# Kernel tuning notes

Hardware: AMD Instinct MI355X
Metric: run time of the kernel (lower is better)

Reference implementation:

```python
import jax, jax.numpy as jnp
import numpy as np
import math

N = 2048          # rows (forced: input_dim_B // 2)
DB = 4096         # input_dim_B
DA = 5120         # input_dim_A
DX2 = DA - DB     # 1024, X2 feature dim
M1, M2 = 8, 4
DK, DV1, DV2 = 64, 64, 64
M = 512           # d_model of trailing encoder layers (nhead=1 inside)
LN_EPS = 1e-5


def setup_inputs() -> dict:
    key = jax.random.key(0)
    ks = jax.random.split(key, 24)
    s = 0.02
    f32 = jnp.float32
    inp = {
        "X1": jax.random.normal(ks[0], (N, DB), f32),
        "X2": jax.random.normal(ks[1], (N, DX2), f32),
        "X3": jax.random.normal(ks[2], (N, DB), f32),
        # Type-A heads (stacked over m1)
        "WQ": jax.random.normal(ks[3], (M1, DA, DK), f32) * s,
        "WK": jax.random.normal(ks[4], (M1, DA, DK), f32) * s,
        "WV": jax.random.normal(ks[5], (M1, DA, DV1), f32) * s,
        # Type-B heads (stacked over m2)
        "WVB": jax.random.normal(ks[6], (M2, DX2, DV2), f32) * s,
        "W_ali": jax.random.normal(ks[7], (DB, DB // 2), f32) * s,
        "W_O": jax.random.normal(ks[8], (M1 * DV1 + M2 * DV2, M), f32) * s,
        # two TransformerEncoderLayers (post-LN, nhead=1, relu FFN), stacked over layer dim
        "enc_Wq": jax.random.normal(ks[9], (2, M, M), f32) * s,
        "enc_Wk": jax.random.normal(ks[10], (2, M, M), f32) * s,
        "enc_Wv": jax.random.normal(ks[11], (2, M, M), f32) * s,
        "enc_bq": jnp.zeros((2, M), f32),
        "enc_bk": jnp.zeros((2, M), f32),
        "enc_bv": jnp.zeros((2, M), f32),
        "enc_Wo": jax.random.normal(ks[12], (2, M, M), f32) * s,
        "enc_bo": jnp.zeros((2, M), f32),
        "enc_ln1_g": jnp.ones((2, M), f32),
        "enc_ln1_b": jnp.zeros((2, M), f32),
        "enc_W1": jax.random.normal(ks[13], (2, M, DV1), f32) * s,
        "enc_b1": jnp.zeros((2, DV1), f32),
        "enc_W2": jax.random.normal(ks[14], (2, DV1, M), f32) * s,
        "enc_b2": jnp.zeros((2, M), f32),
        "enc_ln2_g": jnp.ones((2, M), f32),
        "enc_ln2_b": jnp.zeros((2, M), f32),
    }
    return inp


def _layer_norm(x, g, b):
    mu = jnp.mean(x, axis=-1, keepdims=True)
    var = jnp.mean(jnp.square(x - mu), axis=-1, keepdims=True)
    return (x - mu) * jax.lax.rsqrt(var + LN_EPS) * g + b


def _encoder_layer(x, Wq, bq, Wk, bk, Wv, bv, Wo, bo, g1, b1, W1, bW1, W2, bW2, g2, b2):
    # post-norm TransformerEncoderLayer, nhead=1, dropout in eval mode (off)
    q = x @ Wq + bq
    k = x @ Wk + bk
    v = x @ Wv + bv
    att = jax.nn.softmax((q @ k.T) / math.sqrt(M), axis=-1) @ v
    x = _layer_norm(x + (att @ Wo + bo), g1, b1)
    f = jax.nn.relu(x @ W1 + bW1) @ W2 + bW2
    return _layer_norm(x + f, g2, b2)


def reference(X1, X2, X3, WQ, WK, WV, WVB, W_ali, W_O,
              enc_Wq, enc_bq, enc_Wk, enc_bk, enc_Wv, enc_bv, enc_Wo, enc_bo,
              enc_ln1_g, enc_ln1_b, enc_W1, enc_b1, enc_W2, enc_b2, enc_ln2_g, enc_ln2_b):
    XA = jnp.concatenate([X1, X2], axis=1)  # [N, DA]
    # Type-A heads, batched over m1
    Q = jnp.einsum('nd,hdk->hnk', XA, WQ)
    K = jnp.einsum('nd,hdk->hnk', XA, WK)
    V = jnp.einsum('nd,hdv->hnv', XA, WV)
    scores = jnp.einsum('hnk,hmk->hnm', Q, K) / math.sqrt(DK)
    S = jax.nn.softmax(scores, axis=1)  # torch softmax(dim=0): over query/row axis
    ZA = jnp.einsum('hnm,hmv->hnv', S, V)             # [m1, N, dv1]
    ZA = jnp.transpose(ZA, (1, 0, 2)).reshape(N, M1 * DV1)
    # Type-B heads
    ali = jax.nn.sigmoid(X3) @ W_ali                  # [N, N] (DB//2 == N)
    zb = jnp.einsum('nd,hdv->hnv', X2, WVB)           # [m2, N, dv2]
    ZB = jnp.einsum('nm,hmv->hnv', ali, zb)
    ZB = jnp.transpose(ZB, (1, 0, 2)).reshape(N, M2 * DV2)
    Z = jnp.concatenate([ZA, ZB], axis=1) @ W_O       # [N, M]
    for l in range(2):
        Z = _encoder_layer(Z, enc_Wq[l], enc_bq[l], enc_Wk[l], enc_bk[l],
                           enc_Wv[l], enc_bv[l], enc_Wo[l], enc_bo[l],
                           enc_ln1_g[l], enc_ln1_b[l], enc_W1[l], enc_b1[l],
                           enc_W2[l], enc_b2[l], enc_ln2_g[l], enc_ln2_b[l])
    return Z
```

## Files before the change

### kernel.cpp

```cpp
#include <hip/hip_runtime.h>

#define DEV __device__ __forceinline__

typedef __attribute__((ext_vector_type(4))) float f32x4;
typedef __attribute__((ext_vector_type(8))) short s16x8;

DEV ushort f2b(float f) {
  union { float f; unsigned u; } x; x.f = f;
  unsigned r = (x.u + 0x7FFFu + ((x.u >> 16) & 1u)) >> 16;
  return (ushort)r;
}
DEV float b2f(ushort u) {
  union { unsigned u; float f; } x; x.u = ((unsigned)u) << 16;
  return x.f;
}

DEV void gload16(const ushort* g, ushort* l) {
  __builtin_amdgcn_global_load_lds(
      (const __attribute__((address_space(1))) unsigned int*)g,
      (__attribute__((address_space(3))) unsigned int*)l, 16, 0, 0);
}

struct PtrList { const float* p[4]; };

template<int BM, int BN, int BIAS, int ACT, bool OF, bool OB, int SKX,
         bool CSTAT, bool RSTAT, int NBUF>
__global__ __launch_bounds__(256) void gemm(
    const ushort* __restrict__ A, int lda, long long sA,
    const ushort* __restrict__ B, int ldb, long long sB,
    float* __restrict__ Cf, ushort* __restrict__ Cb, int ldc, long long sC,
    const float* __restrict__ bias, const float* __restrict__ bias2,
    float* __restrict__ pmo, float* __restrict__ pso,
    float scale0, float scale1, int K)
{
  constexpr int WM = BM / 2, WN = BN / 2, FM = WM / 16, FN = WN / 16;
  __shared__ __align__(16) ushort As[NBUF][BM * 64];
  __shared__ __align__(16) ushort Bs[NBUF][BN * 64];
  const int tid = threadIdx.x, l = tid & 63, w = tid >> 6;
  const int wr = w >> 1, wc = w & 1;
  const int gx = gridDim.x, gy = gridDim.y;
  const int nwg = gx * gy;
  const int orig = blockIdx.y * gx + blockIdx.x;
  const int xcd = orig & 7, rest = orig >> 3;
  const int q8 = nwg >> 3, r8 = nwg & 7;
  const int f = (xcd < r8 ? xcd * (q8 + 1) : r8 * (q8 + 1) + (xcd - r8) * q8) + rest;
  int bxr = f / gy;
  const int byy = f - bxr * gy;
  int ks = 0;
  if constexpr (SKX > 1) {
    const int nbx = gx / SKX;
    ks = bxr / nbx; bxr -= ks * nbx;
  }
  const int brow = byy * BM, bcol = bxr * BN;
  const long long z = blockIdx.z;
  A += z * sA + (size_t)ks * K;
  B += z * sB + (size_t)ks * K;
  const int lr = l & 15;
  const int sw = lr & 7, kh = l >> 4;
  f32x4 acc[FM][FN] = {};
  const int nk = K >> 6;

  auto stage = [&](int kt, int buf) {
    const int kof = kt << 6;
#pragma unroll
    for (int i = 0; i < BM / 32; ++i) {
      const int c = i * 256 + tid;
      const int r = c >> 3, k8 = c & 7;
      gload16(A + (size_t)(brow + r) * lda + kof + ((k8 ^ (r & 7)) << 3),
              &As[buf][i * 2048 + w * 512]);
    }
#pragma unroll
    for (int i = 0; i < BN / 32; ++i) {
      const int c = i * 256 + tid;
      const int r = c >> 3, k8 = c & 7;
      gload16(B + (size_t)(bcol + r) * ldb + kof + ((k8 ^ (r & 7)) << 3),
              &Bs[buf][i * 2048 + w * 512]);
    }
  };

  auto compute = [&](int kt, int buf) {
#pragma unroll
    for (int kk = 0; kk < 2; ++kk) {
      const int koff = ((kk * 4 + kh) ^ sw) << 3;
      s16x8 af[FM], bf[FN];
#pragma unroll
      for (int m = 0; m < FM; ++m)
        af[m] = *(const s16x8*)&As[buf][(wr * WM + m * 16 + lr) * 64 + koff];
#pragma unroll
      for (int n = 0; n < FN; ++n)
        bf[n] = *(const s16x8*)&Bs[buf][(wc * WN + n * 16 + lr) * 64 + koff];
#pragma unroll
      for (int m = 0; m < FM; ++m)
#pragma unroll
        for (int n = 0; n < FN; ++n)
          acc[m][n] = __builtin_amdgcn_mfma_f32_16x16x32_bf16(af[m], bf[n], acc[m][n], 0, 0, 0);
    }
  };

  if constexpr (NBUF == 2) {
    stage(0, 0);
    __syncthreads();
    for (int kt = 0; kt < nk - 1; ++kt) {
      stage(kt + 1, (kt + 1) & 1);
      compute(kt, kt & 1);
      __syncthreads();
    }
    compute(nk - 1, (nk - 1) & 1);
  } else {
    for (int kt = 0; kt < nk; ++kt) {
      stage(kt, 0);
      __syncthreads();
      compute(kt, 0);
      __syncthreads();
    }
  }

  if constexpr (OF || OB) {
    const float sc = (z == 0) ? scale0 : scale1;
    const float* bp = (z == 0) ? bias : bias2;
    const int cr = (l >> 4) * 4, cc = l & 15;
#pragma unroll
    for (int m = 0; m < FM; ++m) {
      const int r0 = brow + wr * WM + m * 16 + cr;
#pragma unroll
      for (int n = 0; n < FN; ++n) {
        const int gc = bcol + wc * WN + n * 16 + cc;
        float bc = 0.f;
        if constexpr (BIAS == 1) bc = bp[gc];
#pragma unroll
        for (int j = 0; j < 4; ++j) {
          float v = acc[m][n][j];
          if constexpr (BIAS == 1) v += bc;
          if constexpr (BIAS == 2) v += bp[r0 + j];
          v *= sc;
          if constexpr (ACT == 1) v = fmaxf(v, 0.f);
          const size_t off = (size_t)(r0 + j) * ldc + gc + (size_t)((z * SKX + ks) * sC);
          if constexpr (OF) Cf[off] = v;
          if constexpr (OB) Cb[off] = f2b(v);
        }
      }
    }
  }

  if constexpr (CSTAT) {
    __shared__ float sM[2][2][FN][16], sS[2][2][FN][16];
    float mx[FN], se[FN];
#pragma unroll
    for (int n = 0; n < FN; ++n) {
      float m0 = -3e38f;
#pragma unroll
      for (int m = 0; m < FM; ++m)
#pragma unroll
        for (int j = 0; j < 4; ++j) m0 = fmaxf(m0, acc[m][n][j]);
      float s0 = 0.f;
#pragma unroll
      for (int m = 0; m < FM; ++m)
#pragma unroll
        for (int j = 0; j < 4; ++j) s0 += __expf(acc[m][n][j] - m0);
      mx[n] = m0; se[n] = s0;
    }
#pragma unroll
    for (int o = 16; o <= 32; o <<= 1) {
#pragma unroll
      for (int n = 0; n < FN; ++n) {
        float m2 = __shfl_xor(mx[n], o), s2 = __shfl_xor(se[n], o);
        float M = fmaxf(mx[n], m2);
        se[n] = se[n] * __expf(mx[n] - M) + s2 * __expf(m2 - M);
        mx[n] = M;
      }
    }
    __syncthreads();
    if (l < 16) {
#pragma unroll
      for (int n = 0; n < FN; ++n) { sM[wr][wc][n][l] = mx[n]; sS[wr][wc][n][l] = se[n]; }
    }
    __syncthreads();
    if (wr == 0 && l < 16) {
#pragma unroll
      for (int n = 0; n < FN; ++n) {
        float m1 = sM[0][wc][n][l], m2 = sM[1][wc][n][l];
        float s1 = sS[0][wc][n][l], s2 = sS[1][wc][n][l];
        float M = fmaxf(m1, m2);
        float S = s1 * __expf(m1 - M) + s2 * __expf(m2 - M);
        const int gc = bcol + wc * 32 + n * 16 + l;
        const size_t o = ((size_t)(z * gy + byy)) * 2048 + gc;
        pmo[o] = M; pso[o] = S;
      }
    }
  }

  if constexpr (RSTAT) {
    __shared__ float sRM[2][2][WM], sRS[2][2][WM];
#pragma unroll
    for (int m = 0; m < FM; ++m) {
#pragma unroll
      for (int j = 0; j < 4; ++j) {
        float m0 = -3e38f;
#pragma unroll
        for (int n = 0; n < FN; ++n) m0 = fmaxf(m0, acc[m][n][j]);
        float s0 = 0.f;
#pragma unroll
        for (int n = 0; n < FN; ++n) s0 += __expf(acc[m][n][j] - m0);
#pragma unroll
        for (int o = 1; o <= 8; o <<= 1) {
          float m2 = __shfl_xor(m0, o), s2 = __shfl_xor(s0, o);
          float M = fmaxf(m0, m2);
          s0 = s0 * __expf(m0 - M) + s2 * __expf(m2 - M);
          m0 = M;
        }
        if ((l & 15) == 0) {
          sRM[wr][wc][m * 16 + (l >> 4) * 4 + j] = m0;
          sRS[wr][wc][m * 16 + (l >> 4) * 4 + j] = s0;
        }
      }
    }
    __syncthreads();
    if (wc == 0) {
      float m1 = sRM[wr][0][l], m2 = sRM[wr][1][l];
      float s1 = sRS[wr][0][l], s2 = sRS[wr][1][l];
      float M = fmaxf(m1, m2);
      float S = s1 * __expf(m1 - M) + s2 * __expf(m2 - M);
      const size_t o = (size_t)bxr * 2048 + brow + wr * WM + l;
      pmo[o] = M; pso[o] = S;
    }
  }
}

struct Frag8 { int dummy; };

template<int MH, int NH, bool RA, bool RB>
DEV void phase_read(const ushort* __restrict__ Asb, const ushort* __restrict__ Bsb,
                    int arow, int brw, int kh, int sw,
                    s16x8 (&af)[2][4], s16x8 (&bfh)[2][2][2]) {
  if constexpr (RA) {
#pragma unroll
    for (int kk = 0; kk < 2; ++kk) {
      const int koff = ((kk * 4 + kh) ^ sw) << 3;
#pragma unroll
      for (int m = 0; m < 4; ++m)
        af[kk][m] = *(const s16x8*)&Asb[MH * 8192 + (arow + m * 16) * 64 + koff];
    }
  }
  if constexpr (RB) {
#pragma unroll
    for (int kk = 0; kk < 2; ++kk) {
      const int koff = ((kk * 4 + kh) ^ sw) << 3;
#pragma unroll
      for (int n = 0; n < 2; ++n)
        bfh[NH][kk][n] = *(const s16x8*)&Bsb[NH * 8192 + (brw + n * 16) * 64 + koff];
    }
  }
}

template<int MH, int NH>
DEV void qmfma(const s16x8 (&af)[2][4], const s16x8 (&bfh)[2][2][2],
               f32x4 (&acc)[8][4]) {
#pragma unroll
  for (int kk = 0; kk < 2; ++kk)
#pragma unroll
    for (int m = 0; m < 4; ++m)
#pragma unroll
      for (int n = 0; n < 2; ++n)
        acc[MH * 4 + m][NH * 2 + n] = __builtin_amdgcn_mfma_f32_16x16x32_bf16(
            af[kk][m], bfh[NH][kk][n], acc[MH * 4 + m][NH * 2 + n], 0, 0, 0);
}

DEV void tailwait(int c) {
  if (c == 1) { asm volatile("s_waitcnt vmcnt(4)" ::: "memory"); }
  else if (c == 2) { asm volatile("s_waitcnt vmcnt(0)" ::: "memory"); }
}

template<int NBX>
__global__ __launch_bounds__(512, 2) void gemm256(
    const ushort* __restrict__ A, int lda,
    const ushort* __restrict__ B, int ldb,
    ushort* __restrict__ Cb, int ldc, long long sC, int Kc)
{
  __shared__ __align__(16) ushort As[2][2][8192];
  __shared__ __align__(16) ushort Bs[2][2][8192];
  const int tid = threadIdx.x, l = tid & 63, w = tid >> 6;
  const int wr = w >> 2, wc = w & 3;
  const int gx = gridDim.x, gy = gridDim.y;
  const int nwg = gx * gy;
  const int orig = blockIdx.y * gx + blockIdx.x;
  const int xcd = orig & 7, rest = orig >> 3;
  const int q8 = nwg >> 3, r8 = nwg & 7;
  const int f = (xcd < r8 ? xcd * (q8 + 1) : r8 * (q8 + 1) + (xcd - r8) * q8) + rest;
  int bxr = f / gy;
  const int byy = f - bxr * gy;
  const int ks = bxr / NBX; bxr -= ks * NBX;
  const int brow = byy * 256, bcol = bxr * 256;
  A += (size_t)ks * Kc;
  B += (size_t)ks * Kc;
  const int nk = Kc >> 6;
  const int lr = l & 15, kh = l >> 4, sw = lr & 7;
  const int arow = wr * 64 + lr, brw = wc * 32 + lr;

  const int r0 = tid >> 3, k80 = tid & 7;
  const size_t aoff = (size_t)(brow + r0) * lda + ((k80 ^ (r0 & 7)) << 3);
  const size_t boff = (size_t)(bcol + r0) * ldb + ((k80 ^ (r0 & 7)) << 3);

  f32x4 acc[8][4] = {};
  s16x8 af[2][4];
  s16x8 bfh[2][2][2];

  auto stA = [&](int kt, int buf, int half) {
    if (kt >= nk) return;
    const ushort* s = A + aoff + (size_t)(half * 128) * lda + (kt << 6);
    gload16(s, &As[buf][half][w * 512]);
    gload16(s + (size_t)64 * lda, &As[buf][half][4096 + w * 512]);
  };
  auto stB = [&](int kt, int buf, int half) {
    if (kt >= nk) return;
    const ushort* s = B + boff + (size_t)(half * 128) * ldb + (kt << 6);
    gload16(s, &Bs[buf][half][w * 512]);
    gload16(s + (size_t)64 * ldb, &Bs[buf][half][4096 + w * 512]);
  };

  stA(0, 0, 0); stB(0, 0, 0); stA(0, 0, 1); stB(0, 0, 1);
  stA(1, 1, 0); stB(1, 1, 0);
  asm volatile("s_waitcnt vmcnt(4)" ::: "memory");
  asm volatile("s_barrier" ::: "memory");

#define PH(BUF, MH, NH, RA, RB, STG, TW) do {                                  \
    phase_read<MH, NH, RA, RB>(&As[BUF][0][0], &Bs[BUF][0][0],                 \
                               arow, brw, kh, sw, af, bfh);                    \
    STG;                                                                       \
    asm volatile("s_barrier" ::: "memory");                                    \
    asm volatile("s_waitcnt lgkmcnt(0)" ::: "memory");                         \
    __builtin_amdgcn_sched_barrier(0);                                         \
    __builtin_amdgcn_s_setprio(1);                                             \
    qmfma<MH, NH>(af, bfh, acc);                                               \
    __builtin_amdgcn_s_setprio(0);                                             \
    tailwait(TW);                                                              \
    asm volatile("s_barrier" ::: "memory");                                    \
  } while (0)

  const int NT2 = nk >> 1;
#pragma unroll 1
  for (int j = 0; j < NT2; ++j) {
    const int t1 = 2 * j + 1, t2 = 2 * j + 2, t3 = 2 * j + 3;
    const int tw4 = (t2 < nk) ? 1 : 2;
    const int tw8 = (t2 < nk) ? 1 : 0;
    PH(0, 0, 0, true,  true,  stA(t1, 1, 1), 0);
    PH(0, 0, 1, false, true,  stB(t1, 1, 1), 0);
    PH(0, 1, 0, true,  false, stA(t2, 0, 0), 0);
    PH(0, 1, 1, false, false, stB(t2, 0, 0), tw4);
    PH(1, 0, 0, true,  true,  stA(t2, 0, 1), 0);
    PH(1, 0, 1, false, true,  stB(t2, 0, 1), 0);
    PH(1, 1, 0, true,  false, stA(t3, 1, 0), 0);
    PH(1, 1, 1, false, false, stB(t3, 1, 0), tw8);
  }
#undef PH

  ushort* out = Cb + (size_t)ks * sC;
  const int cr = kh * 4, cc = lr;
#pragma unroll
  for (int mh = 0; mh < 2; ++mh)
#pragma unroll
    for (int m = 0; m < 4; ++m) {
      const int ro = brow + mh * 128 + wr * 64 + m * 16 + cr;
#pragma unroll
      for (int nh = 0; nh < 2; ++nh)
#pragma unroll
        for (int n = 0; n < 2; ++n) {
          const int gc = bcol + nh * 128 + wc * 32 + n * 16 + cc;
#pragma unroll
          for (int j2 = 0; j2 < 4; ++j2)
            out[(size_t)(ro + j2) * ldc + gc] = f2b(acc[mh * 4 + m][nh * 2 + n][j2]);
        }
    }
}

__global__ __launch_bounds__(256) void ffn_fused(
    const ushort* __restrict__ X, const ushort* __restrict__ W1,
    const float* __restrict__ b1, const ushort* __restrict__ W2T,
    const float* __restrict__ b2, float* __restrict__ Y)
{
  __shared__ __align__(16) ushort As[64 * 64];
  __shared__ __align__(16) ushort Bs[64 * 64];
  __shared__ __align__(16) ushort Hs[64 * 64];
  const int tid = threadIdx.x, l = tid & 63, w = tid >> 6;
  const int wr = w >> 1, wc = w & 1;
  const int bx = blockIdx.x, brow = blockIdx.y * 64;
  const int lr = l & 15, g = l >> 4, sw = lr & 7;
  f32x4 acc[2][2] = {};
  for (int kt = 0; kt < 8; ++kt) {
    const int kof = kt << 6;
#pragma unroll
    for (int i = 0; i < 2; ++i) {
      const int c = i * 256 + tid, r = c >> 3, k8 = c & 7;
      gload16(X + (size_t)(brow + r) * 512 + kof + ((k8 ^ (r & 7)) << 3),
              &As[i * 2048 + w * 512]);
    }
#pragma unroll
    for (int i = 0; i < 2; ++i) {
      const int c = i * 256 + tid, r = c >> 3, k8 = c & 7;
      gload16(W1 + (size_t)r * 512 + kof + ((k8 ^ (r & 7)) << 3),
              &Bs[i * 2048 + w * 512]);
    }
    __syncthreads();
#pragma unroll
    for (int kk = 0; kk < 2; ++kk) {
      const int koff = ((kk * 4 + g) ^ sw) << 3;
      s16x8 af[2], bf[2];
#pragma unroll
      for (int m = 0; m < 2; ++m) af[m] = *(const s16x8*)&As[(wr * 32 + m * 16 + lr) * 64 + koff];
#pragma unroll
      for (int n = 0; n < 2; ++n) bf[n] = *(const s16x8*)&Bs[(wc * 32 + n * 16 + lr) * 64 + koff];
#pragma unroll
      for (int m = 0; m < 2; ++m)
#pragma unroll
        for (int n = 0; n < 2; ++n)
          acc[m][n] = __builtin_amdgcn_mfma_f32_16x16x32_bf16(af[m], bf[n], acc[m][n], 0, 0, 0);
    }
    __syncthreads();
  }
#pragma unroll
  for (int m = 0; m < 2; ++m)
#pragma unroll
    for (int n = 0; n < 2; ++n) {
      const int col = wc * 32 + n * 16 + lr;
      const float bb = b1[col];
#pragma unroll
      for (int j = 0; j < 4; ++j) {
        const int row = wr * 32 + m * 16 + g * 4 + j;
        Hs[row * 64 + (((col >> 3) ^ (row & 7)) << 3) + (col & 7)] =
            f2b(fmaxf(acc[m][n][j] + bb, 0.f));
      }
    }
#pragma unroll
  for (int i = 0; i < 2; ++i) {
    const int c = i * 256 + tid, r = c >> 3, k8 = c & 7;
    gload16(W2T + (size_t)(bx * 64 + r) * 64 + ((k8 ^ (r & 7)) << 3),
            &Bs[i * 2048 + w * 512]);
  }
  __syncthreads();
  f32x4 acc2[2][2] = {};
#pragma unroll
  for (int kk = 0; kk < 2; ++kk) {
    const int koff = ((kk * 4 + g) ^ sw) << 3;
    s16x8 af[2], bf[2];
#pragma unroll
    for (int m = 0; m < 2; ++m) af[m] = *(const s16x8*)&Hs[(wr * 32 + m * 16 + lr) * 64 + koff];
#pragma unroll
    for (int n = 0; n < 2; ++n) bf[n] = *(const s16x8*)&Bs[(wc * 32 + n * 16 + lr) * 64 + koff];
#pragma unroll
    for (int m = 0; m < 2; ++m)
#pragma unroll
      for (int n = 0; n < 2; ++n)
        acc2[m][n] = __builtin_amdgcn_mfma_f32_16x16x32_bf16(af[m], bf[n], acc2[m][n], 0, 0, 0);
  }
#pragma unroll
  for (int m = 0; m < 2; ++m)
#pragma unroll
    for (int n = 0; n < 2; ++n) {
      const int gc = bx * 64 + wc * 32 + n * 16 + lr;
      const float bb = b2[gc];
#pragma unroll
      for (int j = 0; j < 4; ++j) {
        const int row = brow + wr * 32 + m * 16 + g * 4 + j;
        Y[(size_t)row * 512 + gc] = acc2[m][n][j] + bb;
      }
    }
}

__global__ __launch_bounds__(256) void pv_fused(
    const ushort* __restrict__ Q, const ushort* __restrict__ K,
    const ushort* __restrict__ Vt, const float* __restrict__ lse,
    ushort* __restrict__ ZAP)
{
  __shared__ __align__(16) ushort Qs[64 * 64];
  __shared__ __align__(16) ushort Ks[2][64 * 64];
  __shared__ __align__(16) ushort Vs[2][64 * 64];
  __shared__ __align__(16) ushort Ps[64 * 64];
  __shared__ float Ls[512];
  const int tid = threadIdx.x, l = tid & 63, w = tid >> 6;
  const int wr = w >> 1, wc = w & 1;
  const int h = blockIdx.z, brow = blockIdx.x * 64, ms = blockIdx.y;
  const int lr = l & 15, g = l >> 4, sw = lr & 7;

  auto stageKV = [&](int mc, int buf) {
#pragma unroll
    for (int i = 0; i < 2; ++i) {
      const int c = i * 256 + tid, r = c >> 3, k8 = c & 7;
      gload16(K + (size_t)(mc * 64 + r) * 512 + h * 64 + ((k8 ^ (r & 7)) << 3),
              &Ks[buf][i * 2048 + w * 512]);
    }
#pragma unroll
    for (int i = 0; i < 2; ++i) {
      const int c = i * 256 + tid, r = c >> 3, k8 = c & 7;
      gload16(Vt + (size_t)(h * 64 + r) * 2048 + mc * 64 + ((k8 ^ (r & 7)) << 3),
              &Vs[buf][i * 2048 + w * 512]);
    }
  };

#pragma unroll
  for (int i = 0; i < 2; ++i) {
    const int c = i * 256 + tid, r = c >> 3, k8 = c & 7;
    gload16(Q + (size_t)(brow + r) * 512 + h * 64 + ((k8 ^ (r & 7)) << 3),
            &Qs[i * 2048 + w * 512]);
  }
  stageKV(ms * 8, 0);
  for (int i = tid; i < 512; i += 256) Ls[i] = lse[h * 2048 + ms * 512 + i];
  __syncthreads();

  s16x8 aq[2][2];
#pragma unroll
  for (int nf = 0; nf < 2; ++nf)
#pragma unroll
    for (int kk = 0; kk < 2; ++kk)
      aq[nf][kk] = *(const s16x8*)&Qs[(wr * 32 + nf * 16 + lr) * 64 + (((kk * 4 + g) ^ sw) << 3)];

  f32x4 zacc[2][2] = {};
  for (int mi = 0; mi < 8; ++mi) {
    const int mc = ms * 8 + mi;
    const int buf = mi & 1;
    if (mi < 7) stageKV(mc + 1, buf ^ 1);
    f32x4 sacc[2][2] = {};
#pragma unroll
    for (int kk = 0; kk < 2; ++kk) {
      const int koff = ((kk * 4 + g) ^ sw) << 3;
      s16x8 bk[2];
#pragma unroll
      for (int mf = 0; mf < 2; ++mf)
        bk[mf] = *(const s16x8*)&Ks[buf][(wc * 32 + mf * 16 + lr) * 64 + koff];
#pragma unroll
      for (int nf = 0; nf < 2; ++nf)
#pragma unroll
        for (int mf = 0; mf < 2; ++mf)
          sacc[nf][mf] = __builtin_amdgcn_mfma_f32_16x16x32_bf16(aq[nf][kk], bk[mf], sacc[nf][mf], 0, 0, 0);
    }
#pragma unroll
    for (int nf = 0; nf < 2; ++nf)
#pragma unroll
      for (int mf = 0; mf < 2; ++mf) {
        const int m_loc = wc * 32 + mf * 16 + lr;
        const float lv = Ls[mi * 64 + m_loc];
#pragma unroll
        for (int j = 0; j < 4; ++j) {
          const int n_loc = wr * 32 + nf * 16 + g * 4 + j;
          Ps[n_loc * 64 + (((m_loc >> 3) ^ (n_loc & 7)) << 3) + (m_loc & 7)] =
              f2b(__expf(sacc[nf][mf][j] - lv));
        }
      }
    __syncthreads();
#pragma unroll
    for (int kk = 0; kk < 2; ++kk) {
      const int koff = ((kk * 4 + g) ^ sw) << 3;
      s16x8 pa[2], bv[2];
#pragma unroll
      for (int nf = 0; nf < 2; ++nf)
        pa[nf] = *(const s16x8*)&Ps[(wr * 32 + nf * 16 + lr) * 64 + koff];
#pragma unroll
      for (int vf = 0; vf < 2; ++vf)
        bv[vf] = *(const s16x8*)&Vs[buf][(wc * 32 + vf * 16 + lr) * 64 + koff];
#pragma unroll
      for (int nf = 0; nf < 2; ++nf)
#pragma unroll
        for (int vf = 0; vf < 2; ++vf)
          zacc[nf][vf] = __builtin_amdgcn_mfma_f32_16x16x32_bf16(pa[nf], bv[vf], zacc[nf][vf], 0, 0, 0);
    }
    __syncthreads();
  }
  ushort* out = ZAP + (size_t)ms * 2048 * 512;
#pragma unroll
  for (int nf = 0; nf < 2; ++nf)
#pragma unroll
    for (int vf = 0; vf < 2; ++vf)
#pragma unroll
      for (int j = 0; j < 4; ++j) {
        const int n = brow + wr * 32 + nf * 16 + g * 4 + j;
        const int col = h * 64 + wc * 32 + vf * 16 + lr;
        out[(size_t)n * 512 + col] = f2b(zacc[nf][vf][j]);
      }
}

template<int NS, int ACT>
__global__ __launch_bounds__(256) void reduceN(const ushort* __restrict__ P, long long sC,
    ushort* __restrict__ out, int cols, int ldout, long long zPoff, long long zOoff,
    int cshift, long long bstride, float scale, int scThresh, int rows,
    const float* __restrict__ bias)
{
  P += blockIdx.z * zPoff; out += blockIdx.z * zOoff;
  const int c4n = cols >> 2;
  const size_t total = (size_t)rows * c4n;
  for (size_t i = (size_t)blockIdx.x * 256 + threadIdx.x; i < total; i += (size_t)gridDim.x * 256) {
    const size_t r = i / c4n;
    const int c4 = (int)(i - r * c4n) << 2;
    float4 s = make_float4(0.f, 0.f, 0.f, 0.f);
#pragma unroll
    for (int k = 0; k < NS; ++k) {
      ushort4 t = *(const ushort4*)(P + (size_t)k * sC + r * cols + c4);
      s.x += b2f(t.x); s.y += b2f(t.y); s.z += b2f(t.z); s.w += b2f(t.w);
    }
    if constexpr (ACT == 1) {
      float4 bb = *(const float4*)(bias + c4);
      s.x = fmaxf(s.x + bb.x, 0.f); s.y = fmaxf(s.y + bb.y, 0.f);
      s.z = fmaxf(s.z + bb.z, 0.f); s.w = fmaxf(s.w + bb.w, 0.f);
    }
    const float sc = (c4 < scThresh) ? scale : 1.f;
    ushort4 o;
    o.x = f2b(s.x * sc); o.y = f2b(s.y * sc); o.z = f2b(s.z * sc); o.w = f2b(s.w * sc);
    const size_t oo = r * ldout + (size_t)(c4 >> cshift) * bstride + (c4 & ((1 << cshift) - 1));
    *(ushort4*)(out + oo) = o;
  }
}

__global__ __launch_bounds__(256) void prep_xab(const float* __restrict__ X1,
    const float* __restrict__ X2, ushort* __restrict__ XAb) {
  const size_t total = (size_t)2048 * 1280;
  for (size_t i = (size_t)blockIdx.x * 256 + threadIdx.x; i < total; i += (size_t)gridDim.x * 256) {
    const size_t r = i / 1280;
    const int c = (int)(i - r * 1280) << 2;
    float4 v = (c < 4096) ? *(const float4*)(X1 + r * 4096 + c)
                          : *(const float4*)(X2 + r * 1024 + (c - 4096));
    ushort4 o; o.x = f2b(v.x); o.y = f2b(v.y); o.z = f2b(v.z); o.w = f2b(v.w);
    *(ushort4*)(XAb + r * 5120 + c) = o;
  }
}

__global__ __launch_bounds__(256) void prep_x3w(const float* __restrict__ X3,
    const float* __restrict__ Wali, ushort* __restrict__ sX3,
    ushort* __restrict__ Walib) {
  const size_t n1 = (size_t)2048 * 1024;
  const size_t n2 = (size_t)4096 * 512;
  const size_t total = n1 + n2;
  for (size_t i = (size_t)blockIdx.x * 256 + threadIdx.x; i < total; i += (size_t)gridDim.x * 256) {
    if (i < n1) {
      const size_t r = i / 1024;
      const int c = (int)(i - r * 1024) << 2;
      float4 v = *(const float4*)(X3 + r * 4096 + c);
      v.x = 1.f / (1.f + __expf(-v.x)); v.y = 1.f / (1.f + __expf(-v.y));
      v.z = 1.f / (1.f + __expf(-v.z)); v.w = 1.f / (1.f + __expf(-v.w));
      ushort4 o; o.x = f2b(v.x); o.y = f2b(v.y); o.z = f2b(v.z); o.w = f2b(v.w);
      *(ushort4*)(sX3 + r * 4096 + c) = o;
    } else {
      const size_t j = i - n1;
      const size_t r = j / 512;
      const int c = (int)(j - r * 512) << 2;
      float4 v = *(const float4*)(Wali + r * 2048 + c);
      ushort4 o; o.x = f2b(v.x); o.y = f2b(v.y); o.z = f2b(v.z); o.w = f2b(v.w);
      *(ushort4*)(Walib + r * 2048 + c) = o;
    }
  }
}

__global__ __launch_bounds__(256) void expconv_row(const float* __restrict__ S,
    const float* __restrict__ pm, const float* __restrict__ ps, ushort* __restrict__ P) {
  const int r = blockIdx.x;
  float m = pm[(size_t)(threadIdx.x & 31) * 2048 + r];
  float s = ps[(size_t)(threadIdx.x & 31) * 2048 + r];
#pragma unroll
  for (int o = 1; o < 32; o <<= 1) {
    float m2 = __shfl_xor(m, o), s2 = __shfl_xor(s, o);
    float M = fmaxf(m, m2);
    s = s * __expf(m - M) + s2 * __expf(m2 - M);
    m = M;
  }
  const float L = m + __logf(s);
  const float* row = S + (size_t)r * 2048;
  ushort* pr = P + (size_t)r * 2048;
  for (int c = threadIdx.x * 4; c < 2048; c += 1024) {
    float4 v = *(const float4*)(row + c);
    ushort4 o4;
    o4.x = f2b(__expf(v.x - L)); o4.y = f2b(__expf(v.y - L));
    o4.z = f2b(__expf(v.z - L)); o4.w = f2b(__expf(v.w - L));
    *(ushort4*)(pr + c) = o4;
  }
}

__global__ __launch_bounds__(256) void colcombine(const float* __restrict__ pm,
    const float* __restrict__ ps, float* __restrict__ lse) {
  const int id = blockIdx.x * 256 + threadIdx.x;
  const int h = id >> 11, c = id & 2047;
  float M = -3e38f;
#pragma unroll
  for (int s = 0; s < 16; ++s) M = fmaxf(M, pm[((size_t)(h * 16 + s)) * 2048 + c]);
  float S = 0.f;
#pragma unroll
  for (int s = 0; s < 16; ++s) {
    size_t o = ((size_t)(h * 16 + s)) * 2048 + c;
    S += ps[o] * __expf(pm[o] - M);
  }
  lse[id] = M + __logf(S);
}

__global__ __launch_bounds__(256) void transpose_conv_multi(PtrList in, int zPerT,
    ushort* __restrict__ out, int R, int C) {
  __shared__ ushort t[32][33];
  const int z = blockIdx.z;
  const float* ip = in.p[z / zPerT] + (size_t)(z % zPerT) * R * C;
  ushort* op = out + (size_t)z * R * C;
  const int r0 = blockIdx.x * 32, c0 = blockIdx.y * 32;
#pragma unroll
  for (int i = 0; i < 4; ++i) {
    int r = r0 + threadIdx.y + i * 8;
    int c = c0 + threadIdx.x;
    float v = (r < R && c < C) ? ip[(size_t)r * C + c] : 0.f;
    t[threadIdx.x][threadIdx.y + i * 8] = f2b(v);
  }
  __syncthreads();
#pragma unroll
  for (int i = 0; i < 4; ++i) {
    int c = c0 + threadIdx.y + i * 8;
    int r = r0 + threadIdx.x;
    if (c < C && r < R) op[(size_t)c * R + r] = t[threadIdx.y + i * 8][threadIdx.x];
  }
}

__global__ __launch_bounds__(256) void transpose_conv_batch(
    const float* __restrict__ WVB, ushort* __restrict__ WVBT,
    const float* __restrict__ W_O, ushort* __restrict__ WOT,
    const float* __restrict__ eW1, ushort* __restrict__ EW1T,
    const float* __restrict__ eW2, ushort* __restrict__ EW2T) {
  __shared__ ushort t[32][33];
  const int b = blockIdx.x;
  const float* ip; ushort* op; int R, C, r0, c0;
  if (b < 256) {
    const int h = b >> 6, loc = b & 63;
    ip = WVB + (size_t)h * 65536; op = WVBT + (size_t)h * 65536;
    R = 1024; C = 64; r0 = (loc & 31) * 32; c0 = (loc >> 5) * 32;
  } else if (b < 640) {
    const int loc = b - 256;
    ip = W_O; op = WOT;
    R = 768; C = 512; r0 = (loc % 24) * 32; c0 = (loc / 24) * 32;
  } else if (b < 704) {
    const int loc = b - 640, lyr = loc >> 5, lo = loc & 31;
    ip = eW1 + (size_t)lyr * 32768; op = EW1T + (size_t)lyr * 32768;
    R = 512; C = 64; r0 = (lo & 15) * 32; c0 = (lo >> 4) * 32;
  } else {
    const int loc = b - 704, lyr = loc >> 5, lo = loc & 31;
    ip = eW2 + (size_t)lyr * 32768; op = EW2T + (size_t)lyr * 32768;
    R = 64; C = 512; r0 = (lo & 1) * 32; c0 = (lo >> 1) * 32;
  }
#pragma unroll
  for (int i = 0; i < 4; ++i) {
    int r = r0 + threadIdx.y + i * 8;
    int c = c0 + threadIdx.x;
    float v = (r < R && c < C) ? ip[(size_t)r * C + c] : 0.f;
    t[threadIdx.x][threadIdx.y + i * 8] = f2b(v);
  }
  __syncthreads();
#pragma unroll
  for (int i = 0; i < 4; ++i) {
    int c = c0 + threadIdx.y + i * 8;
    int r = r0 + threadIdx.x;
    if (c < C && r < R) op[(size_t)c * R + r] = t[threadIdx.y + i * 8][threadIdx.x];
  }
}

__global__ __launch_bounds__(256) void transpose_b16(const ushort* __restrict__ in,
    ushort* __restrict__ out, int R, int C) {
  __shared__ ushort t[32][33];
  const int r0 = blockIdx.x * 32, c0 = blockIdx.y * 32;
#pragma unroll
  for (int i = 0; i < 4; ++i)
    t[threadIdx.x][threadIdx.y + i * 8] = in[(size_t)(r0 + threadIdx.y + i * 8) * C + c0 + threadIdx.x];
  __syncthreads();
#pragma unroll
  for (int i = 0; i < 4; ++i)
    out[(size_t)(c0 + threadIdx.y + i * 8) * R + r0 + threadIdx.x] = t[threadIdx.y + i * 8][threadIdx.x];
}

__global__ __launch_bounds__(256) void ln_add(const float* __restrict__ X,
    const float* __restrict__ Y, const float* __restrict__ g, const float* __restrict__ b,
    float* __restrict__ of, ushort* __restrict__ ob) {
  const int r = blockIdx.x, t = threadIdx.x;
  const size_t base = (size_t)r * 512;
  float v0 = X[base + t] + Y[base + t];
  float v1 = X[base + t + 256] + Y[base + t + 256];
  float s = v0 + v1;
#pragma unroll
  for (int o = 1; o < 64; o <<= 1) s += __shfl_xor(s, o);
  __shared__ float sm[4], sq[4];
  const int l = t & 63, w = t >> 6;
  if (l == 0) sm[w] = s;
  __syncthreads();
  const float mu = (sm[0] + sm[1] + sm[2] + sm[3]) * (1.f / 512.f);
  const float d0 = v0 - mu, d1 = v1 - mu;
  float q = d0 * d0 + d1 * d1;
#pragma unroll
  for (int o = 1; o < 64; o <<= 1) q += __shfl_xor(q, o);
  if (l == 0) sq[w] = q;
  __syncthreads();
  const float var = (sq[0] + sq[1] + sq[2] + sq[3]) * (1.f / 512.f);
  const float rs = rsqrtf(var + 1e-5f);
  const float o0 = d0 * rs * g[t] + b[t];
  const float o1 = d1 * rs * g[t + 256] + b[t + 256];
  if (of) { of[base + t] = o0; of[base + t + 256] = o1; }
  if (ob) { ob[base + t] = f2b(o0); ob[base + t + 256] = f2b(o1); }
}

extern "C" void kernel_launch(void* const* d_in, const int* in_sizes, int n_in,
                              void* d_out, int out_size, void* d_ws, size_t ws_size,
                              hipStream_t stream) {
  (void)in_sizes; (void)n_in; (void)out_size;
  const float* X1   = (const float*)d_in[0];
  const float* X2   = (const float*)d_in[1];
  const float* X3   = (const float*)d_in[2];
  const float* WQ   = (const float*)d_in[3];
  const float* WK   = (const float*)d_in[4];
  const float* WV   = (const float*)d_in[5];
  const float* WVB  = (const float*)d_in[6];
  const float* Wali = (const float*)d_in[7];
  const float* W_O  = (const float*)d_in[8];
  const float* eWq  = (const float*)d_in[9];
  const float* eWk  = (const float*)d_in[10];
  const float* eWv  = (const float*)d_in[11];
  const float* ebq  = (const float*)d_in[12];
  const float* ebk  = (const float*)d_in[13];
  const float* ebv  = (const float*)d_in[14];
  const float* eWo  = (const float*)d_in[15];
  const float* ebo  = (const float*)d_in[16];
  const float* eg1  = (const float*)d_in[17];
  const float* ebl1 = (const float*)d_in[18];
  const float* eW1  = (const float*)d_in[19];
  const float* eB1  = (const float*)d_in[20];
  const float* eW2  = (const float*)d_in[21];
  const float* eB2  = (const float*)d_in[22];
  const float* eg2  = (const float*)d_in[23];
  const float* ebl2 = (const float*)d_in[24];
  float* OUT = (float*)d_out;
  char* ws = (char*)d_ws;

  const size_t oQB   = 0;
  const size_t oKB   = 2097152;
  const size_t oVB   = 4194304;
  const size_t oVTB  = 6291456;
  const size_t oZAB  = 8388608;
  const size_t oWOT  = 11534336;
  const size_t oEWQT = 12320768;
  const size_t oEWVT = 14417920;
  const size_t oEWOT = 15466496;
  const size_t oEW1T = 16515072;
  const size_t oEW2T = 16646144;
  const size_t oWVBT = 16777216;
  const size_t oZBT  = 17301504;
  const size_t oZ    = 18350080;
  const size_t oZB16 = 22544384;
  const size_t oX2F  = 24641536;
  const size_t oX2B  = 28835840;
  const size_t oY    = 30932992;
  const size_t oATT  = 35127296;
  const size_t oPM   = 37486592;
  const size_t oPS   = 38535168;
  const size_t oLSE  = 39583744;
  const size_t oDYN  = 39649280;
  const size_t oWQT  = oDYN;
  const size_t oQKVP = oDYN + 15728640;
  const size_t oZBP  = oDYN;
  const size_t oSX3  = oDYN;
  const size_t oWAB  = oDYN + 16777216;
  const size_t oW2P  = oDYN + 33554432;
  const size_t oW2T  = oDYN + 50331648;
  const size_t oZAP  = oDYN;
  const size_t oSCFe = oDYN;
  const size_t oPbe  = oDYN + 16777216;
  const size_t oATTP = oDYN + 50331648;
  if (ws_size < oDYN + 67108864) return;

  ushort* XAb  = (ushort*)(ws + oZ);
  ushort* WQT  = (ushort*)(ws + oWQT);
  ushort* QKVP = (ushort*)(ws + oQKVP);
  ushort* ZBP  = (ushort*)(ws + oZBP);
  ushort* sX3  = (ushort*)(ws + oSX3);
  ushort* Walib= (ushort*)(ws + oWAB);
  ushort* W2P  = (ushort*)(ws + oW2P);
  ushort* W2Tb = (ushort*)(ws + oW2T);
  ushort* ZBP2 = (ushort*)(ws + oW2P);
  ushort* ZAP  = (ushort*)(ws + oZAP);
  float*  SCFe = (float*)(ws + oSCFe);
  ushort* Pbe  = (ushort*)(ws + oPbe);
  ushort* ATTP = (ushort*)(ws + oATTP);
  ushort* Qb   = (ushort*)(ws + oQB);
  ushort* Kb   = (ushort*)(ws + oKB);
  ushort* Vb   = (ushort*)(ws + oVB);
  ushort* Vtb  = (ushort*)(ws + oVTB);
  ushort* ZABb = (ushort*)(ws + oZAB);
  ushort* WOT  = (ushort*)(ws + oWOT);
  ushort* EWQT = (ushort*)(ws + oEWQT);
  ushort* EWVT = (ushort*)(ws + oEWVT);
  ushort* EWOT = (ushort*)(ws + oEWOT);
  ushort* EW1T = (ushort*)(ws + oEW1T);
  ushort* EW2T = (ushort*)(ws + oEW2T);
  ushort* WVBT = (ushort*)(ws + oWVBT);
  ushort* ZBT  = (ushort*)(ws + oZBT);
  float*  Zf   = (float*)(ws + oZ);
  ushort* Zb16 = (ushort*)(ws + oZB16);
  float*  X2f  = (float*)(ws + oX2F);
  ushort* X2b  = (ushort*)(ws + oX2B);
  float*  Yf   = (float*)(ws + oY);
  ushort* ATTb = (ushort*)(ws + oATT);
  float*  PM   = (float*)(ws + oPM);
  float*  PS   = (float*)(ws + oPS);
  float*  LSE  = (float*)(ws + oLSE);

  const dim3 tb(32, 8);
  const float rs512 = 0.044194173824159216f;

  prep_xab<<<2048, 256, 0, stream>>>(X1, X2, XAb);
  {
    PtrList wqkv; wqkv.p[0] = WQ; wqkv.p[1] = WK; wqkv.p[2] = WV; wqkv.p[3] = nullptr;
    transpose_conv_multi<<<dim3(160, 2, 24), tb, 0, stream>>>(wqkv, 8, WQT, 5120, 64);
    PtrList enc4; enc4.p[0] = eWq; enc4.p[1] = eWk; enc4.p[2] = eWv; enc4.p[3] = eWo;
    transpose_conv_multi<<<dim3(16, 16, 8), tb, 0, stream>>>(enc4, 2, EWQT, 512, 512);
  }
  transpose_conv_batch<<<768, tb, 0, stream>>>(WVB, WVBT, W_O, WOT, eW1, EW1T, eW2, EW2T);

  gemm256<6><<<dim3(30, 8, 1), 512, 0, stream>>>(
      XAb, 5120, WQT, 5120, QKVP, 1536, 3145728LL, 1024);
  reduceN<5,0><<<1024, 256, 0, stream>>>(QKVP, 3145728LL, Qb, 1536, 512, 0, 0,
      9, 1048576LL, 0.125f, 512, 2048, nullptr);
  transpose_b16<<<dim3(64, 16), tb, 0, stream>>>(Vb, Vtb, 2048, 512);
  gemm<64,64,0,0,false,true,4,false,false,1><<<dim3(128,4,1), 256, 0, stream>>>(
      WVBT, 1024, 0, XAb + 4096, 5120, 0, nullptr, ZBP, 2048, 524288LL,
      nullptr, nullptr, nullptr, nullptr, 1.f, 1.f, 256);
  reduceN<4,0><<<1024, 256, 0, stream>>>(ZBP, 524288LL, ZBT, 2048, 2048, 0, 0,
      30, 0, 1.f, 0, 256, nullptr);

  prep_x3w<<<2048, 256, 0, stream>>>(X3, Wali, sX3, Walib);
  gemm<128,128,0,0,false,true,4,false,false,2><<<dim3(128,2,1), 256, 0, stream>>>(
      ZBT, 2048, 0, Walib, 2048, 0, nullptr, W2P, 4096, 1048576LL,
      nullptr, nullptr, nullptr, nullptr, 1.f, 1.f, 512);
  reduceN<4,0><<<512, 256, 0, stream>>>(W2P, 1048576LL, W2Tb, 4096, 4096, 0, 0,
      30, 0, 1.f, 0, 256, nullptr);
  gemm<128,64,0,0,false,true,8,false,false,1><<<dim3(32,16,1), 256, 0, stream>>>(
      sX3, 4096, 0, W2Tb, 4096, 0, nullptr, ZBP2, 256, 524288LL,
      nullptr, nullptr, nullptr, nullptr, 1.f, 1.f, 512);
  reduceN<8,0><<<512, 256, 0, stream>>>(ZBP2, 524288LL, ZABb + 512, 256, 768, 0, 0,
      30, 0, 1.f, 0, 2048, nullptr);

  gemm<128,64,0,0,false,false,1,true,false,1><<<dim3(32,16,8), 256, 0, stream>>>(
      Qb, 512, 64, Kb, 512, 64, nullptr, nullptr, 2048, 0,
      nullptr, nullptr, PM, PS, 1.f, 1.f, 64);
  colcombine<<<64, 256, 0, stream>>>(PM, PS, LSE);
  pv_fused<<<dim3(32, 4, 8), 256, 0, stream>>>(Qb, Kb, Vtb, LSE, ZAP);
  reduceN<4,0><<<1024, 256, 0, stream>>>(ZAP, 1048576LL, ZABb, 512, 768, 0, 0,
      30, 0, 1.f, 0, 2048, nullptr);

  gemm<64,64,0,0,true,true,1,false,false,2><<<dim3(8,32,1), 256, 0, stream>>>(
      ZABb, 768, 0, WOT, 768, 0, Zf, Zb16, 512, 0,
      nullptr, nullptr, nullptr, nullptr, 1.f, 1.f, 768);

  for (int lyr = 0; lyr < 2; ++lyr) {
    const ushort* wq = EWQT + (size_t)lyr * 262144;
    const ushort* wv = EWVT + (size_t)lyr * 262144;
    const ushort* wo = EWOT + (size_t)lyr * 262144;
    const ushort* w1 = EW1T + (size_t)lyr * 32768;
    const ushort* w2 = EW2T + (size_t)lyr * 32768;
    gemm<128,64,1,0,false,true,1,false,false,2><<<dim3(8,16,2), 256, 0, stream>>>(
        Zb16, 512, 0, wq, 512, 524288LL, nullptr, Qb, 512, 1048576LL,
        ebq + lyr * 512, ebk + lyr * 512, nullptr, nullptr, rs512, 1.f, 512);
    gemm<64,64,2,0,false,true,1,false,false,2><<<dim3(32,8,1), 256, 0, stream>>>(
        wv, 512, 0, Zb16, 512, 0, nullptr, Vtb, 2048, 0,
        ebv + lyr * 512, nullptr, nullptr, nullptr, 1.f, 1.f, 512);
    gemm<128,64,0,0,true,false,1,false,true,1><<<dim3(32,16,1), 256, 0, stream>>>(
        Qb, 512, 0, Kb, 512, 0, SCFe, nullptr, 2048, 0,
        nullptr, nullptr, PM, PS, 1.f, 1.f, 512);
    expconv_row<<<2048, 256, 0, stream>>>(SCFe, PM, PS, Pbe);
    gemm<128,64,0,0,false,true,4,false,false,1><<<dim3(32,16,1), 256, 0, stream>>>(
        Pbe, 2048, 0, Vtb, 2048, 0, nullptr, ATTP, 512, 1048576LL,
        nullptr, nullptr, nullptr, nullptr, 1.f, 1.f, 512);
    reduceN<4,0><<<1024, 256, 0, stream>>>(ATTP, 1048576LL, ATTb, 512, 512, 0, 0,
        30, 0, 1.f, 0, 2048, nullptr);
    gemm<64,64,1,0,true,false,1,false,false,2><<<dim3(8,32,1), 256, 0, stream>>>(
        ATTb, 512, 0, wo, 512, 0, Yf, nullptr, 512, 0,
        ebo + lyr * 512, nullptr, nullptr, nullptr, 1.f, 1.f, 512);
    ln_add<<<2048, 256, 0, stream>>>(Zf, Yf, eg1 + lyr * 512, ebl1 + lyr * 512, X2f, X2b);
    ffn_fused<<<dim3(8, 32), 256, 0, stream>>>(
        X2b, w1, eB1 + lyr * 64, w2, eB2 + lyr * 512, Yf);
    ln_add<<<2048, 256, 0, stream>>>(X2f, Yf, eg2 + lyr * 512, ebl2 + lyr * 512,
                                     (lyr == 0) ? Zf : OUT, (lyr == 0) ? Zb16 : nullptr);
  }
}
```

Before: 354.6 us.

## Restructure gemm256 main loop to prefetch LDS fragments ahead of MFMA phases

Replaces the macro-driven eight-phase loop with an explicit schedule that issues the next phase's LDS reads (A and second B half) before or alongside the current phase's MFMAs. Separate register sets for both B halves are kept, and the next tile's first fragments are read at the end of each iteration. The goal is to overlap LDS read latency with matrix compute rather than serializing reads and MFMA inside each phase. In exchange it uses more registers, which could pressure occupancy under launch_bounds(512,2), and it makes the barrier and waitcnt ordering more fragile.

```diff
diff --git a/kernel.cpp b/kernel.cpp
--- a/kernel.cpp
+++ b/kernel.cpp
@@ -226,35 +226,8 @@
   }
 }
 
-struct Frag8 { int dummy; };
-
-template<int MH, int NH, bool RA, bool RB>
-DEV void phase_read(const ushort* __restrict__ Asb, const ushort* __restrict__ Bsb,
-                    int arow, int brw, int kh, int sw,
-                    s16x8 (&af)[2][4], s16x8 (&bfh)[2][2][2]) {
-  if constexpr (RA) {
-#pragma unroll
-    for (int kk = 0; kk < 2; ++kk) {
-      const int koff = ((kk * 4 + kh) ^ sw) << 3;
-#pragma unroll
-      for (int m = 0; m < 4; ++m)
-        af[kk][m] = *(const s16x8*)&Asb[MH * 8192 + (arow + m * 16) * 64 + koff];
-    }
-  }
-  if constexpr (RB) {
-#pragma unroll
-    for (int kk = 0; kk < 2; ++kk) {
-      const int koff = ((kk * 4 + kh) ^ sw) << 3;
-#pragma unroll
-      for (int n = 0; n < 2; ++n)
-        bfh[NH][kk][n] = *(const s16x8*)&Bsb[NH * 8192 + (brw + n * 16) * 64 + koff];
-    }
-  }
-}
-
 template<int MH, int NH>
-DEV void qmfma(const s16x8 (&af)[2][4], const s16x8 (&bfh)[2][2][2],
-               f32x4 (&acc)[8][4]) {
+DEV void qmfma2(const s16x8 (&Ax)[8], const s16x8 (&Bf)[4], f32x4 (&acc)[8][4]) {
 #pragma unroll
   for (int kk = 0; kk < 2; ++kk)
 #pragma unroll
@@ -262,13 +235,17 @@
 #pragma unroll
       for (int n = 0; n < 2; ++n)
         acc[MH * 4 + m][NH * 2 + n] = __builtin_amdgcn_mfma_f32_16x16x32_bf16(
-            af[kk][m], bfh[NH][kk][n], acc[MH * 4 + m][NH * 2 + n], 0, 0, 0);
+            Ax[kk * 4 + m], Bf[kk * 2 + n], acc[MH * 4 + m][NH * 2 + n], 0, 0, 0);
 }
 
 DEV void tailwait(int c) {
   if (c == 1) { asm volatile("s_waitcnt vmcnt(4)" ::: "memory"); }
   else if (c == 2) { asm volatile("s_waitcnt vmcnt(0)" ::: "memory"); }
 }
+
+#define GBAR() asm volatile("s_barrier" ::: "memory")
+#define GLGKM0() do { asm volatile("s_waitcnt lgkmcnt(0)" ::: "memory"); \
+                      __builtin_amdgcn_sched_barrier(0); } while (0)
 
 template<int NBX>
 __global__ __launch_bounds__(512, 2) void gemm256(
@@ -301,8 +278,8 @@
   const size_t boff = (size_t)(bcol + r0) * ldb + ((k80 ^ (r0 & 7)) << 3);
 
   f32x4 acc[8][4] = {};
-  s16x8 af[2][4];
-  s16x8 bfh[2][2][2];
+  s16x8 Ax[8];
+  s16x8 B0s[4], B1s[4];
 
   auto stA = [&](int kt, int buf, int half) {
     if (kt >= nk) return;
@@ -316,42 +293,67 @@
     gload16(s, &Bs[buf][half][w * 512]);
     gload16(s + (size_t)64 * ldb, &Bs[buf][half][4096 + w * 512]);
   };
+  auto rdA = [&](int buf, int half) {
+#pragma unroll
+    for (int kk = 0; kk < 2; ++kk) {
+      const int koff = ((kk * 4 + kh) ^ sw) << 3;
+#pragma unroll
+      for (int m = 0; m < 4; ++m)
+        Ax[kk * 4 + m] = *(const s16x8*)&As[buf][half][(arow + m * 16) * 64 + koff];
+    }
+  };
+  auto rdB = [&](s16x8 (&dst)[4], int buf, int half) {
+#pragma unroll
+    for (int kk = 0; kk < 2; ++kk) {
+      const int koff = ((kk * 4 + kh) ^ sw) << 3;
+#pragma unroll
+      for (int n = 0; n < 2; ++n)
+        dst[kk * 2 + n] = *(const s16x8*)&Bs[buf][half][(brw + n * 16) * 64 + koff];
+    }
+  };
 
   stA(0, 0, 0); stB(0, 0, 0); stA(0, 0, 1); stB(0, 0, 1);
   stA(1, 1, 0); stB(1, 1, 0);
   asm volatile("s_waitcnt vmcnt(4)" ::: "memory");
-  asm volatile("s_barrier" ::: "memory");
-
-#define PH(BUF, MH, NH, RA, RB, STG, TW) do {                                  \
-    phase_read<MH, NH, RA, RB>(&As[BUF][0][0], &Bs[BUF][0][0],                 \
-                               arow, brw, kh, sw, af, bfh);                    \
-    STG;                                                                       \
-    asm volatile("s_barrier" ::: "memory");                                    \
-    asm volatile("s_waitcnt lgkmcnt(0)" ::: "memory");                         \
-    __builtin_amdgcn_sched_barrier(0);                                         \
-    __builtin_amdgcn_s_setprio(1);                                             \
-    qmfma<MH, NH>(af, bfh, acc);                                               \
-    __builtin_amdgcn_s_setprio(0);                                             \
-    tailwait(TW);                                                              \
-    asm volatile("s_barrier" ::: "memory");                                    \
-  } while (0)
+  GBAR();
+  rdA(0, 0); rdB(B0s, 0, 0);
 
   const int NT2 = nk >> 1;
 #pragma unroll 1
   for (int j = 0; j < NT2; ++j) {
-    const int t1 = 2 * j + 1, t2 = 2 * j + 2, t3 = 2 * j + 3;
-    const int tw4 = (t2 < nk) ? 1 : 2;
-    const int tw8 = (t2 < nk) ? 1 : 0;
-    PH(0, 0, 0, true,  true,  stA(t1, 1, 1), 0);
-    PH(0, 0, 1, false, true,  stB(t1, 1, 1), 0);
-    PH(0, 1, 0, true,  false, stA(t2, 0, 0), 0);
-    PH(0, 1, 1, false, false, stB(t2, 0, 0), tw4);
-    PH(1, 0, 0, true,  true,  stA(t2, 0, 1), 0);
-    PH(1, 0, 1, false, true,  stB(t2, 0, 1), 0);
-    PH(1, 1, 0, true,  false, stA(t3, 1, 0), 0);
-    PH(1, 1, 1, false, false, stB(t3, 1, 0), tw8);
-  }
-#undef PH
+    const int tb = 2 * j + 1, ta2 = 2 * j + 2, tb2 = 2 * j + 3;
+    const bool more = (ta2 < nk);
+    stA(tb, 1, 1); GBAR(); GLGKM0();
+    rdB(B1s, 0, 1); __builtin_amdgcn_sched_barrier(0);
+    __builtin_amdgcn_s_setprio(1); qmfma2<0, 0>(Ax, B0s, acc); __builtin_amdgcn_s_setprio(0);
+    GBAR();
+    stB(tb, 1, 1); GBAR(); GLGKM0();
+    __builtin_amdgcn_s_setprio(1); qmfma2<0, 1>(Ax, B1s, acc); __builtin_amdgcn_s_setprio(0);
+    GBAR();
+    stA(ta2, 0, 0); GBAR(); GLGKM0();
+    rdA(0, 1); GLGKM0();
+    __builtin_amdgcn_s_setprio(1); qmfma2<1, 0>(Ax, B0s, acc); __builtin_amdgcn_s_setprio(0);
+    GBAR();
+    stB(ta2, 0, 0); GBAR(); GLGKM0();
+    __builtin_amdgcn_s_setprio(1); qmfma2<1, 1>(Ax, B1s, acc); __builtin_amdgcn_s_setprio(0);
+    tailwait(more ? 1 : 2); GBAR();
+    rdA(1, 0); rdB(B0s, 1, 0);
+    stA(ta2, 0, 1); GBAR(); GLGKM0();
+    rdB(B1s, 1, 1); __builtin_amdgcn_sched_barrier(0);
+    __builtin_amdgcn_s_setprio(1); qmfma2<0, 0>(Ax, B0s, acc); __builtin_amdgcn_s_setprio(0);
+    GBAR();
+    stB(ta2, 0, 1); GBAR(); GLGKM0();
+    __builtin_amdgcn_s_setprio(1); qmfma2<0, 1>(Ax, B1s, acc); __builtin_amdgcn_s_setprio(0);
+    GBAR();
+    stA(tb2, 1, 0); GBAR(); GLGKM0();
+    rdA(1, 1); GLGKM0();
+    __builtin_amdgcn_s_setprio(1); qmfma2<1, 0>(Ax, B0s, acc); __builtin_amdgcn_s_setprio(0);
+    GBAR();
+    stB(tb2, 1, 0); GBAR(); GLGKM0();
+    __builtin_amdgcn_s_setprio(1); qmfma2<1, 1>(Ax, B1s, acc); __builtin_amdgcn_s_setprio(0);
+    tailwait(more ? 1 : 0); GBAR();
+    if (more) { rdA(0, 0); rdB(B0s, 0, 0); }
+  }
 
   ushort* out = Cb + (size_t)ks * sC;
   const int cr = kh * 4, cc = lr;
```

Result: no change. 354.2 us (-0.1%).
